# Optimization experiments

Measured on AMD Instinct MI355X. Metric: run time of the kernel, lower is better.

## Reference

```python
import jax, jax.numpy as jnp
import numpy as np

N, E, G = 20000, 320000, 64
IN, ED, H, F, FC, NC = 6, 2, 4, 64, 64, 2
HF = H * F


def _glorot(key, shape):
    fan_in, fan_out = shape[0], shape[-1]
    s = jnp.sqrt(6.0 / (fan_in + fan_out))
    return jax.random.uniform(key, shape, jnp.float32, -s, s)


def setup_inputs() -> dict:
    key = jax.random.key(0)
    ks = jax.random.split(key, 24)
    inp = {
        "x": jax.random.normal(ks[0], (N, IN), jnp.float32),
        "edge_index": jax.random.randint(ks[1], (2, E), 0, N, jnp.int64),
        "edge_attr": jax.random.normal(ks[2], (E, ED), jnp.float32),
        "batch": jnp.sort(jax.random.randint(ks[3], (N,), 0, G, jnp.int64)),
        # layer 0 (GATv2, in=6 -> 4 heads x 64)
        "Wl0": _glorot(ks[4], (IN, HF)), "bl0": jnp.zeros((HF,), jnp.float32),
        "Wr0": _glorot(ks[5], (IN, HF)), "br0": jnp.zeros((HF,), jnp.float32),
        "We0": _glorot(ks[6], (ED, HF)),
        "att0": _glorot(ks[7], (H, F)), "b0": jnp.zeros((HF,), jnp.float32),
        "proj0": _glorot(ks[8], (IN, HF)),  # residual projection 6 -> 256
        # layer 1 (GATv2, in=256 -> 4 heads x 64); residual is identity (256==256)
        "Wl1": _glorot(ks[9], (HF, HF)), "bl1": jnp.zeros((HF,), jnp.float32),
        "Wr1": _glorot(ks[10], (HF, HF)), "br1": jnp.zeros((HF,), jnp.float32),
        "We1": _glorot(ks[11], (ED, HF)),
        "att1": _glorot(ks[12], (H, F)), "b1": jnp.zeros((HF,), jnp.float32),
        # head
        "Wp": _glorot(ks[13], (HF, FC)), "bp": jnp.zeros((FC,), jnp.float32),
        "Wc": _glorot(ks[14], (FC, NC)), "bc": jnp.zeros((NC,), jnp.float32),
    }
    return inp


def _add_self_loops_mean(src, dst, eattr):
    # PyG add_self_loops(fill_value='mean'): self-loop attr = mean of incoming edge_attr
    s = jax.ops.segment_sum(eattr, dst, num_segments=N)
    c = jax.ops.segment_sum(jnp.ones((eattr.shape[0], 1), eattr.dtype), dst, num_segments=N)
    loop_attr = s / jnp.maximum(c, 1.0)
    idx = jnp.arange(N, dtype=src.dtype)
    return (jnp.concatenate([src, idx]), jnp.concatenate([dst, idx]),
            jnp.concatenate([eattr, loop_attr], axis=0))


def _gatv2(x, src, dst, ee, Wl, bl, Wr, br, att, bias):
    # ee: precomputed edge projection [E2, H, F]
    xl = (x @ Wl + bl).reshape(N, H, F)   # source transform
    xr = (x @ Wr + br).reshape(N, H, F)   # target transform
    m = jax.nn.leaky_relu(xl[src] + xr[dst] + ee, 0.2)   # [E2, H, F]
    logits = jnp.einsum('ehf,hf->eh', m, att)            # [E2, H]
    mx = jax.ops.segment_max(logits, dst, num_segments=N)
    ex = jnp.exp(logits - mx[dst])
    den = jax.ops.segment_sum(ex, dst, num_segments=N)
    alpha = ex / den[dst]                                 # scatter-softmax over dst
    out = jax.ops.segment_sum(xl[src] * alpha[:, :, None], dst, num_segments=N)
    return out.reshape(N, HF) + bias


def reference(x, edge_index, edge_attr, batch,
              Wl0, bl0, Wr0, br0, We0, att0, b0, proj0,
              Wl1, bl1, Wr1, br1, We1, att1, b1,
              Wp, bp, Wc, bc):
    src, dst, eattr = _add_self_loops_mean(edge_index[0], edge_index[1], edge_attr)
    # layer 0 (residual: projected input); dropout is a no-op in eval mode
    h = _gatv2(x, src, dst, (eattr @ We0).reshape(-1, H, F), Wl0, bl0, Wr0, br0, att0, b0)
    x1 = jax.nn.elu(h) + x @ proj0
    # layer 1 (residual: identity)
    h = _gatv2(x1, src, dst, (eattr @ We1).reshape(-1, H, F), Wl1, bl1, Wr1, br1, att1, b1)
    x2 = jax.nn.elu(h) + x1
    # pre-pool MLP + global mean pool over graphs + classifier
    z = jax.nn.elu(x2 @ Wp + bp)                           # [N, FC]
    gs = jax.ops.segment_sum(z, batch, num_segments=G)
    gc = jax.ops.segment_sum(jnp.ones((N, 1), z.dtype), batch, num_segments=G)
    pooled = gs / jnp.maximum(gc, 1.0)                     # [G, FC]
    return pooled @ Wc + bc                                # [G, NC]
```

## Files before the change

kernel.cpp:

```cpp
#include <hip/hip_runtime.h>
#include <math.h>

#define NN   20000
#define NE   320000
#define NG   64
#define INF_ 6
#define EDF  2
#define NH   4
#define FD   64
#define HF   256
#define FCD  64
#define NCD  2
#define CAP  64

#define ZB   ((NN + 255) / 256)
#define WCB  512
#define L0B  ((NN + 3) / 4)

typedef short bf16x8 __attribute__((ext_vector_type(8)));
typedef float f32x4  __attribute__((ext_vector_type(4)));

static __device__ __forceinline__ unsigned short f2bf(float f) {
  unsigned u = __float_as_uint(f);
  unsigned r = 0x7fffu + ((u >> 16) & 1u);
  return (unsigned short)((u + r) >> 16);
}
static __device__ __forceinline__ float4 bf2f4(uint2 p) {
  float4 v;
  v.x = __uint_as_float(p.x << 16);
  v.y = __uint_as_float(p.x & 0xffff0000u);
  v.z = __uint_as_float(p.y << 16);
  v.w = __uint_as_float(p.y & 0xffff0000u);
  return v;
}


__global__ __launch_bounds__(256) void k_init(
    int* __restrict__ cnt, float* __restrict__ gpool,
    const float* __restrict__ Wl1, const float* __restrict__ Wr1,
    unsigned short* __restrict__ Wsw,
    const float* __restrict__ x,
    const float* __restrict__ Wl0, const float* __restrict__ bl0,
    const float* __restrict__ Wr0, const float* __restrict__ br0,
    unsigned short* __restrict__ xlb, unsigned short* __restrict__ xrb) {
  int b = blockIdx.x;
  int t = threadIdx.x;
  if (b < ZB) {
    int i = b * 256 + t;
    if (i < NN) cnt[i] = 0;
  } else if (b == ZB) {
    for (int i = t; i < NG * FCD; i += 256) gpool[i] = 0.f;
  } else if (b < ZB + 1 + WCB) {
    int id = (b - ZB - 1) * 256 + t;
    int j = id & 7, lane = (id >> 3) & 63, kk8 = (id >> 9) & 7, ntg = id >> 12;
    int n = ntg * 16 + (lane & 15);
    int k = kk8 * 32 + (lane >> 4) * 8 + j;
    float v = (n < 256) ? Wl1[k * 256 + n] : Wr1[k * 256 + (n - 256)];
    Wsw[id] = f2bf(v);
  } else {
    int w = t >> 6, lane = t & 63;
    int n = (b - ZB - 1 - WCB) * 4 + w;
    if (n >= NN) return;
    int cb = lane << 2;
    float4 al = *(const float4*)&bl0[cb];
    float4 ar = *(const float4*)&br0[cb];
#pragma unroll
    for (int k = 0; k < INF_; ++k) {
      float xv = x[n * INF_ + k];
      float4 wl = *(const float4*)&Wl0[k * HF + cb];
      float4 wr = *(const float4*)&Wr0[k * HF + cb];
      al.x = fmaf(xv, wl.x, al.x); al.y = fmaf(xv, wl.y, al.y);
      al.z = fmaf(xv, wl.z, al.z); al.w = fmaf(xv, wl.w, al.w);
      ar.x = fmaf(xv, wr.x, ar.x); ar.y = fmaf(xv, wr.y, ar.y);
      ar.z = fmaf(xv, wr.z, ar.z); ar.w = fmaf(xv, wr.w, ar.w);
    }
    uint2 pk;
    pk.x = (unsigned)f2bf(al.x) | ((unsigned)f2bf(al.y) << 16);
    pk.y = (unsigned)f2bf(al.z) | ((unsigned)f2bf(al.w) << 16);
    *(uint2*)&xlb[(size_t)n * HF + cb] = pk;
    uint2 pr;
    pr.x = (unsigned)f2bf(ar.x) | ((unsigned)f2bf(ar.y) << 16);
    pr.y = (unsigned)f2bf(ar.z) | ((unsigned)f2bf(ar.w) << 16);
    *(uint2*)&xrb[(size_t)n * HF + cb] = pr;
  }
}


__global__ void k_scatter(const int* __restrict__ ei, const float* __restrict__ ea,
                          int* __restrict__ cnt, uint2* __restrict__ rec) {
  int i = blockIdx.x * blockDim.x + threadIdx.x;
  if (i >= NE) return;
  int s = ei[i], d = ei[NE + i];
  float2 a = *(const float2*)&ea[2 * i];
  int pos = atomicAdd(&cnt[d], 1);
  if (pos < CAP)
    rec[(size_t)d * CAP + pos] = make_uint2((unsigned)(s * 512),
                                            (unsigned)f2bf(a.x) | ((unsigned)f2bf(a.y) << 16));
}


__global__ __launch_bounds__(256) void k_l1_mfma(
    const unsigned short* __restrict__ x1b,
    const unsigned short* __restrict__ Wsw,
    const float* __restrict__ bl, const float* __restrict__ br,
    unsigned short* __restrict__ xlb, unsigned short* __restrict__ xrb) {
  __shared__ unsigned short so[64][264];
  int t = threadIdx.x;
  int row0 = blockIdx.x * 64;
  int w = t >> 6, lane = t & 63;
  int quad = lane >> 4, ln = lane & 15;
  int y = blockIdx.y;
  const float* bias = y ? br : bl;
  unsigned short* dst = y ? xrb : xlb;

  int arow = row0 + w * 16 + ln; if (arow >= NN) arow = NN - 1;
  const unsigned short* aptr = x1b + (size_t)arow * HF + quad * 8;

  f32x4 acc[16];
#pragma unroll
  for (int i = 0; i < 16; ++i) acc[i] = (f32x4){0.f, 0.f, 0.f, 0.f};

  for (int kk8 = 0; kk8 < 8; ++kk8) {
    bf16x8 af = *(const bf16x8*)(aptr + kk8 * 32);
#pragma unroll
    for (int nt = 0; nt < 16; ++nt) {
      bf16x8 bfr = *(const bf16x8*)&Wsw[(size_t)((((y * 16 + nt) * 8 + kk8) * 64) + lane) * 8];
      acc[nt] = __builtin_amdgcn_mfma_f32_16x16x32_bf16(af, bfr, acc[nt], 0, 0, 0);
    }
  }
#pragma unroll
  for (int nt = 0; nt < 16; ++nt) {
    float bv = bias[nt * 16 + ln];
#pragma unroll
    for (int rg = 0; rg < 4; ++rg)
      so[w * 16 + quad * 4 + rg][nt * 16 + ln] = f2bf(acc[nt][rg] + bv);
  }
  __syncthreads();
#pragma unroll
  for (int i = 0; i < 8; ++i) {
    int idx = i * 256 + t;
    int row = idx >> 5, c8 = idx & 31;
    int grow = row0 + row;
    if (grow < NN)
      *(uint4*)&dst[(size_t)grow * HF + c8 * 8] = *(const uint4*)&so[row][c8 * 8];
  }
}


template <bool L0>
__global__ __launch_bounds__(256) void k_agg(
    const unsigned short* __restrict__ xlb, const unsigned short* xrb_,
    const int* __restrict__ cnt, const uint2* __restrict__ rec,
    const float* __restrict__ att, const float* __restrict__ We,
    const float* __restrict__ bias,
    const float* __restrict__ x, const float* __restrict__ proj0,
    unsigned short* __restrict__ x1bout,
    const unsigned short* __restrict__ x1bin, unsigned short* x2bout) {
  int wid = (blockIdx.x * 256 + threadIdx.x) >> 6;
  if (wid >= NN) return;
  int lane = threadIdx.x & 63;
  int n = wid;
  int cb = lane << 2;

  float4 xr4 = bf2f4(*(const uint2*)&xrb_[(size_t)n * HF + cb]);
  float4 at4 = *(const float4*)&att[cb];
  float4 w04 = *(const float4*)&We[cb];
  float4 w14 = *(const float4*)&We[HF + cb];

  int nreal = min(cnt[n], CAP);
  const uint2* recn = rec + (size_t)n * CAP;
  const char* xlbase = (const char*)xlb + (size_t)(cb * 2);

  float a0s = 0.f, a1s = 0.f;
  for (int e = lane; e < nreal; e += 64) {
    uint2 r = recn[e];
    a0s += __uint_as_float(r.y << 16);
    a1s += __uint_as_float(r.y & 0xffff0000u);
  }
#pragma unroll
  for (int o = 32; o; o >>= 1) {
    a0s += __shfl_xor(a0s, o, 64);
    a1s += __shfl_xor(a1s, o, 64);
  }
  float im = 1.0f / fmaxf((float)nreal, 1.0f);
  float a0m = a0s * im, a1m = a1s * im;

  uint2 ps = *(const uint2*)(xlbase + (unsigned)(n * 512));
  float4 vS = bf2f4(ps);
  float tS;
  {
    float4 mm;
    mm.x = vS.x + fmaf(a0m, w04.x, fmaf(a1m, w14.x, xr4.x));
    mm.y = vS.y + fmaf(a0m, w04.y, fmaf(a1m, w14.y, xr4.y));
    mm.z = vS.z + fmaf(a0m, w04.z, fmaf(a1m, w14.z, xr4.z));
    mm.w = vS.w + fmaf(a0m, w04.w, fmaf(a1m, w14.w, xr4.w));
    mm.x = fmaxf(mm.x, 0.2f * mm.x);
    mm.y = fmaxf(mm.y, 0.2f * mm.y);
    mm.z = fmaxf(mm.z, 0.2f * mm.z);
    mm.w = fmaxf(mm.w, 0.2f * mm.w);
    float tt = mm.x * at4.x;
    tt = fmaf(mm.y, at4.y, tt);
    tt = fmaf(mm.z, at4.z, tt);
    tt = fmaf(mm.w, at4.w, tt);
    tt += __shfl_xor(tt, 1, 64);
    tt += __shfl_xor(tt, 2, 64);
    tt += __shfl_xor(tt, 4, 64);
    tt += __shfl_xor(tt, 8, 64);
    tS = tt;
  }
  float den = 1.f;
  float4 acc = vS;

  if (nreal > 0) {
    int lastE = nreal - 1;
    for (int e0 = 0; e0 < nreal; e0 += 4) {
      uint2 r4[4], p4[4];
#pragma unroll
      for (int i = 0; i < 4; ++i)
        r4[i] = recn[min(e0 + i, lastE)];
#pragma unroll
      for (int i = 0; i < 4; ++i)
        p4[i] = *(const uint2*)(xlbase + r4[i].x);

      float t4[4];
#pragma unroll
      for (int i = 0; i < 4; ++i) {
        float4 vC = bf2f4(p4[i]);
        float a0 = __uint_as_float(r4[i].y << 16);
        float a1 = __uint_as_float(r4[i].y & 0xffff0000u);
        float4 mm;
        mm.x = vC.x + fmaf(a0, w04.x, fmaf(a1, w14.x, xr4.x));
        mm.y = vC.y + fmaf(a0, w04.y, fmaf(a1, w14.y, xr4.y));
        mm.z = vC.z + fmaf(a0, w04.z, fmaf(a1, w14.z, xr4.z));
        mm.w = vC.w + fmaf(a0, w04.w, fmaf(a1, w14.w, xr4.w));
        mm.x = fmaxf(mm.x, 0.2f * mm.x);
        mm.y = fmaxf(mm.y, 0.2f * mm.y);
        mm.z = fmaxf(mm.z, 0.2f * mm.z);
        mm.w = fmaxf(mm.w, 0.2f * mm.w);
        float tt = mm.x * at4.x;
        tt = fmaf(mm.y, at4.y, tt);
        tt = fmaf(mm.z, at4.z, tt);
        tt = fmaf(mm.w, at4.w, tt);
        t4[i] = tt;
      }
#pragma unroll
      for (int o = 1; o <= 8; o <<= 1) {
#pragma unroll
        for (int i = 0; i < 4; ++i) t4[i] += __shfl_xor(t4[i], o, 64);
      }
#pragma unroll
      for (int i = 0; i < 4; ++i) {
        float w = (e0 + i <= lastE) ? __expf(fminf(t4[i] - tS, 80.f)) : 0.f;
        float4 vC = bf2f4(p4[i]);
        den += w;
        acc.x = fmaf(w, vC.x, acc.x);
        acc.y = fmaf(w, vC.y, acc.y);
        acc.z = fmaf(w, vC.z, acc.z);
        acc.w = fmaf(w, vC.w, acc.w);
      }
    }
  }

  float inv = 1.0f / den;
  float4 b4 = *(const float4*)&bias[cb];
  float4 o;
  o.x = fmaf(acc.x, inv, b4.x);
  o.y = fmaf(acc.y, inv, b4.y);
  o.z = fmaf(acc.z, inv, b4.z);
  o.w = fmaf(acc.w, inv, b4.w);
  o.x = (o.x > 0.f) ? o.x : expm1f(o.x);
  o.y = (o.y > 0.f) ? o.y : expm1f(o.y);
  o.z = (o.z > 0.f) ? o.z : expm1f(o.z);
  o.w = (o.w > 0.f) ? o.w : expm1f(o.w);

  if (L0) {
    float4 rr = make_float4(0.f, 0.f, 0.f, 0.f);
#pragma unroll
    for (int k = 0; k < INF_; ++k) {
      float xv = x[n * INF_ + k];
      float4 p = *(const float4*)&proj0[k * HF + cb];
      rr.x = fmaf(xv, p.x, rr.x);
      rr.y = fmaf(xv, p.y, rr.y);
      rr.z = fmaf(xv, p.z, rr.z);
      rr.w = fmaf(xv, p.w, rr.w);
    }
    o.x += rr.x; o.y += rr.y; o.z += rr.z; o.w += rr.w;
    uint2 pk;
    pk.x = (unsigned)f2bf(o.x) | ((unsigned)f2bf(o.y) << 16);
    pk.y = (unsigned)f2bf(o.z) | ((unsigned)f2bf(o.w) << 16);
    *(uint2*)&x1bout[(size_t)n * HF + cb] = pk;
  } else {
    float4 x1v = bf2f4(*(const uint2*)&x1bin[(size_t)n * HF + cb]);
    o.x += x1v.x; o.y += x1v.y; o.z += x1v.z; o.w += x1v.w;
    uint2 pk;
    pk.x = (unsigned)f2bf(o.x) | ((unsigned)f2bf(o.y) << 16);
    pk.y = (unsigned)f2bf(o.z) | ((unsigned)f2bf(o.w) << 16);
    *(uint2*)&x2bout[(size_t)n * HF + cb] = pk;
  }
}


__global__ __launch_bounds__(256) void k_pool(
    const unsigned short* __restrict__ x2b, const float* __restrict__ Wp,
    const float* __restrict__ bp, const int* __restrict__ batch,
    float* __restrict__ gpool) {
  __shared__ float xs[32 * HF];
  __shared__ int gid_s[32];
  int t = threadIdx.x;
  int row0 = blockIdx.x * 32;
  const uint4* s4 = (const uint4*)(x2b + (size_t)row0 * HF);
#pragma unroll
  for (int i = 0; i < 4; ++i) {
    int idx = i * 256 + t;
    uint4 p = s4[idx];
    int base = idx * 8;
    float4 lo = bf2f4(make_uint2(p.x, p.y));
    float4 hi = bf2f4(make_uint2(p.z, p.w));
    *(float4*)&xs[base] = lo;
    *(float4*)&xs[base + 4] = hi;
  }
  if (t < 32) gid_s[t] = batch[row0 + t];
  __syncthreads();
  int j = t & 63, rg = t >> 6;
  float acc[8];
#pragma unroll
  for (int rr = 0; rr < 8; ++rr) acc[rr] = 0.f;
  for (int k4 = 0; k4 < HF / 4; ++k4) {
    float w0 = Wp[(k4 * 4 + 0) * FCD + j];
    float w1 = Wp[(k4 * 4 + 1) * FCD + j];
    float w2 = Wp[(k4 * 4 + 2) * FCD + j];
    float w3 = Wp[(k4 * 4 + 3) * FCD + j];
#pragma unroll
    for (int rr = 0; rr < 8; ++rr) {
      float4 xv = *(const float4*)&xs[(rg * 8 + rr) * HF + k4 * 4];
      acc[rr] = fmaf(xv.x, w0, acc[rr]);
      acc[rr] = fmaf(xv.y, w1, acc[rr]);
      acc[rr] = fmaf(xv.z, w2, acc[rr]);
      acc[rr] = fmaf(xv.w, w3, acc[rr]);
    }
  }
  float b = bp[j];
  int gprev = gid_s[rg * 8];
  float run = 0.f;
#pragma unroll
  for (int rr = 0; rr < 8; ++rr) {
    float a = acc[rr] + b;
    float z = (a > 0.f) ? a : expm1f(a);
    int g = gid_s[rg * 8 + rr];
    if (g != gprev) {
      atomicAdd(&gpool[gprev * FCD + j], run);
      run = 0.f; gprev = g;
    }
    run += z;
  }
  atomicAdd(&gpool[gprev * FCD + j], run);
}


__global__ void k_head(const float* __restrict__ gpool, const int* __restrict__ batch,
                       const float* __restrict__ Wc, const float* __restrict__ bc,
                       float* __restrict__ out) {
  int t = threadIdx.x;
  int g = t >> 1, k = t & 1;
  int lo = 0, hi = NN;
  while (lo < hi) { int mid = (lo + hi) >> 1; if (batch[mid] < g) lo = mid + 1; else hi = mid; }
  int c0 = lo;
  lo = 0; hi = NN;
  while (lo < hi) { int mid = (lo + hi) >> 1; if (batch[mid] < g + 1) lo = mid + 1; else hi = mid; }
  int c1 = lo;
  float inv = 1.0f / fmaxf((float)(c1 - c0), 1.0f);
  float a = bc[k];
  for (int j = 0; j < FCD; ++j)
    a = fmaf(gpool[g * FCD + j] * inv, Wc[j * NCD + k], a);
  out[g * NCD + k] = a;
}


extern "C" void kernel_launch(void* const* d_in, const int* in_sizes, int n_in,
                              void* d_out, int out_size, void* d_ws, size_t ws_size,
                              hipStream_t stream) {
  const float* x    = (const float*)d_in[0];
  const int*   ei   = (const int*)d_in[1];
  const float* ea   = (const float*)d_in[2];
  const int*   batch= (const int*)d_in[3];
  const float* Wl0  = (const float*)d_in[4];
  const float* bl0  = (const float*)d_in[5];
  const float* Wr0  = (const float*)d_in[6];
  const float* br0  = (const float*)d_in[7];
  const float* We0  = (const float*)d_in[8];
  const float* att0 = (const float*)d_in[9];
  const float* b0   = (const float*)d_in[10];
  const float* proj0= (const float*)d_in[11];
  const float* Wl1  = (const float*)d_in[12];
  const float* bl1  = (const float*)d_in[13];
  const float* Wr1  = (const float*)d_in[14];
  const float* br1  = (const float*)d_in[15];
  const float* We1  = (const float*)d_in[16];
  const float* att1 = (const float*)d_in[17];
  const float* b1   = (const float*)d_in[18];
  const float* Wp   = (const float*)d_in[19];
  const float* bp   = (const float*)d_in[20];
  const float* Wc   = (const float*)d_in[21];
  const float* bc   = (const float*)d_in[22];
  float* out = (float*)d_out;

  char* ws = (char*)d_ws;
  size_t off = 0;
  int*   cnt    = (int*)(ws + off);   off += (NN * 4 + 15) / 16 * 16;
  uint2* rec    = (uint2*)(ws + off); off += (size_t)NN * CAP * 8;
  unsigned short* xlb = (unsigned short*)(ws + off); off += (size_t)NN * HF * 2;
  unsigned short* xrb = (unsigned short*)(ws + off); off += (size_t)NN * HF * 2;
  unsigned short* x1b = (unsigned short*)(ws + off); off += (size_t)NN * HF * 2;
  float* gpool  = (float*)(ws + off); off += NG * FCD * 4;
  unsigned short* Wsw = (unsigned short*)(ws + off); off += 512 * 256 * 2;
  unsigned short* x2b = xrb;
  (void)ws_size; (void)in_sizes; (void)n_in; (void)out_size;

  k_init<<<ZB + 1 + WCB + L0B, 256, 0, stream>>>(
      cnt, gpool, Wl1, Wr1, Wsw, x, Wl0, bl0, Wr0, br0, xlb, xrb);

  k_scatter<<<(NE + 255) / 256, 256, 0, stream>>>(ei, ea, cnt, rec);

  k_agg<true><<<(NN * 64 + 255) / 256, 256, 0, stream>>>(
      xlb, xrb, cnt, rec, att0, We0, b0, x, proj0, x1b, nullptr, nullptr);

  k_l1_mfma<<<dim3((NN + 63) / 64, 2), 256, 0, stream>>>(x1b, Wsw, bl1, br1, xlb, xrb);
  k_agg<false><<<(NN * 64 + 255) / 256, 256, 0, stream>>>(
      xlb, xrb, cnt, rec, att1, We1, b1, nullptr, nullptr, nullptr, x1b, x2b);

  k_pool<<<NN / 32, 256, 0, stream>>>(x2b, Wp, bp, batch, gpool);
  k_head<<<1, 128, 0, stream>>>(gpool, batch, Wc, bc, out);
}
```

Before: 266.1 us.

## Fuse edge-attr mean into softmax loop, pack FP32 math, count graph sizes in pool

The aggregation kernel no longer makes a separate pass over the edge records to compute the self-loop mean attribute. It accumulates that sum inside the main softmax loop and handles the self-loop term afterwards, which lets the max-shift subtraction be dropped. The edge loop is unrolled from 4 to 8 edges per iteration and uses two-wide float vectors so the compiler can emit packed FP32 instructions, and a dummy early record load is kept alive with an empty asm statement. The pooling kernel now counts nodes per graph with atomics, replacing the binary searches in the head kernel. Dropping the max-shift makes the exponent depend only on the clamp at 80, which risks overflow or precision differences for large logits.

New measurement: 304.4 us. +14.4%, slower.

```diff
diff --git a/kernel.cpp b/kernel.cpp
--- a/kernel.cpp
+++ b/kernel.cpp
@@ -19,6 +19,7 @@
 
 typedef short bf16x8 __attribute__((ext_vector_type(8)));
 typedef float f32x4  __attribute__((ext_vector_type(4)));
+typedef float f32x2  __attribute__((ext_vector_type(2)));
 
 static __device__ __forceinline__ unsigned short f2bf(float f) {
   unsigned u = __float_as_uint(f);
@@ -33,10 +34,16 @@
   v.w = __uint_as_float(p.y & 0xffff0000u);
   return v;
 }
+static __device__ __forceinline__ f32x2 bflo2(unsigned u) {
+  f32x2 v;
+  v.x = __uint_as_float(u << 16);
+  v.y = __uint_as_float(u & 0xffff0000u);
+  return v;
+}
 
 
 __global__ __launch_bounds__(256) void k_init(
-    int* __restrict__ cnt, float* __restrict__ gpool,
+    int* __restrict__ cnt, float* __restrict__ gpool, int* __restrict__ gcnt,
     const float* __restrict__ Wl1, const float* __restrict__ Wr1,
     unsigned short* __restrict__ Wsw,
     const float* __restrict__ x,
@@ -50,6 +57,7 @@
     if (i < NN) cnt[i] = 0;
   } else if (b == ZB) {
     for (int i = t; i < NG * FCD; i += 256) gpool[i] = 0.f;
+    if (t < NG) gcnt[t] = 0;
   } else if (b < ZB + 1 + WCB) {
     int id = (b - ZB - 1) * 256 + t;
     int j = id & 7, lane = (id >> 3) & 63, kk8 = (id >> 9) & 7, ntg = id >> 12;
@@ -161,130 +169,121 @@
   int lane = threadIdx.x & 63;
   int n = wid;
   int cb = lane << 2;
+  unsigned cbb = (unsigned)(cb << 1);
+
+  const char* xlbase = (const char*)xlb;
+  uint2 ps = *(const uint2*)(xlbase + ((unsigned)(n * 512) + cbb));
 
   float4 xr4 = bf2f4(*(const uint2*)&xrb_[(size_t)n * HF + cb]);
   float4 at4 = *(const float4*)&att[cb];
   float4 w04 = *(const float4*)&We[cb];
   float4 w14 = *(const float4*)&We[HF + cb];
+  f32x2 xrA = {xr4.x, xr4.y}, xrB = {xr4.z, xr4.w};
+  f32x2 atA = {at4.x, at4.y}, atB = {at4.z, at4.w};
+  f32x2 w0A = {w04.x, w04.y}, w0B = {w04.z, w04.w};
+  f32x2 w1A = {w14.x, w14.y}, w1B = {w14.z, w14.w};
 
   int nreal = min(cnt[n], CAP);
+  int lastE = nreal - 1;
   const uint2* recn = rec + (size_t)n * CAP;
-  const char* xlbase = (const char*)xlb + (size_t)(cb * 2);
-
-  float a0s = 0.f, a1s = 0.f;
-  for (int e = lane; e < nreal; e += 64) {
-    uint2 r = recn[e];
-    a0s += __uint_as_float(r.y << 16);
-    a1s += __uint_as_float(r.y & 0xffff0000u);
-  }
-#pragma unroll
-  for (int o = 32; o; o >>= 1) {
-    a0s += __shfl_xor(a0s, o, 64);
-    a1s += __shfl_xor(a1s, o, 64);
-  }
+  uint2 pre = recn[lane];
+
+  f32x2 accA = {0.f, 0.f}, accB = {0.f, 0.f};
+  float den = 0.f, a0s = 0.f, a1s = 0.f;
+
+  for (int e0 = 0; e0 < nreal; e0 += 8) {
+    uint2 r8[8], p8[8];
+#pragma unroll
+    for (int i = 0; i < 8; ++i)
+      r8[i] = recn[min(e0 + i, lastE)];
+#pragma unroll
+    for (int i = 0; i < 8; ++i)
+      p8[i] = *(const uint2*)(xlbase + (r8[i].x + cbb));
+
+    float t8[8];
+#pragma unroll
+    for (int i = 0; i < 8; ++i) {
+      float a0 = __uint_as_float(r8[i].y << 16);
+      float a1 = __uint_as_float(r8[i].y & 0xffff0000u);
+      if (e0 + i <= lastE) { a0s += a0; a1s += a1; }
+      f32x2 a0v = {a0, a0}, a1v = {a1, a1};
+      f32x2 mA = a1v * w1A + xrA; mA = a0v * w0A + mA;
+      f32x2 mB = a1v * w1B + xrB; mB = a0v * w0B + mB;
+      mA = mA + bflo2(p8[i].x);
+      mB = mB + bflo2(p8[i].y);
+      mA.x = fmaxf(mA.x, 0.2f * mA.x);
+      mA.y = fmaxf(mA.y, 0.2f * mA.y);
+      mB.x = fmaxf(mB.x, 0.2f * mB.x);
+      mB.y = fmaxf(mB.y, 0.2f * mB.y);
+      f32x2 d = mA * atA;
+      d = mB * atB + d;
+      t8[i] = d.x + d.y;
+    }
+#pragma unroll
+    for (int o = 1; o <= 8; o <<= 1) {
+#pragma unroll
+      for (int i = 0; i < 8; ++i) t8[i] += __shfl_xor(t8[i], o, 64);
+    }
+#pragma unroll
+    for (int i = 0; i < 8; ++i) {
+      float w = (e0 + i <= lastE) ? __expf(fminf(t8[i], 80.f)) : 0.f;
+      den += w;
+      f32x2 wv = {w, w};
+      accA = wv * bflo2(p8[i].x) + accA;
+      accB = wv * bflo2(p8[i].y) + accB;
+    }
+  }
+
   float im = 1.0f / fmaxf((float)nreal, 1.0f);
   float a0m = a0s * im, a1m = a1s * im;
-
-  uint2 ps = *(const uint2*)(xlbase + (unsigned)(n * 512));
-  float4 vS = bf2f4(ps);
-  float tS;
+  f32x2 vSA = bflo2(ps.x), vSB = bflo2(ps.y);
   {
-    float4 mm;
-    mm.x = vS.x + fmaf(a0m, w04.x, fmaf(a1m, w14.x, xr4.x));
-    mm.y = vS.y + fmaf(a0m, w04.y, fmaf(a1m, w14.y, xr4.y));
-    mm.z = vS.z + fmaf(a0m, w04.z, fmaf(a1m, w14.z, xr4.z));
-    mm.w = vS.w + fmaf(a0m, w04.w, fmaf(a1m, w14.w, xr4.w));
-    mm.x = fmaxf(mm.x, 0.2f * mm.x);
-    mm.y = fmaxf(mm.y, 0.2f * mm.y);
-    mm.z = fmaxf(mm.z, 0.2f * mm.z);
-    mm.w = fmaxf(mm.w, 0.2f * mm.w);
-    float tt = mm.x * at4.x;
-    tt = fmaf(mm.y, at4.y, tt);
-    tt = fmaf(mm.z, at4.z, tt);
-    tt = fmaf(mm.w, at4.w, tt);
-    tt += __shfl_xor(tt, 1, 64);
-    tt += __shfl_xor(tt, 2, 64);
-    tt += __shfl_xor(tt, 4, 64);
-    tt += __shfl_xor(tt, 8, 64);
-    tS = tt;
-  }
-  float den = 1.f;
-  float4 acc = vS;
-
-  if (nreal > 0) {
-    int lastE = nreal - 1;
-    for (int e0 = 0; e0 < nreal; e0 += 4) {
-      uint2 r4[4], p4[4];
-#pragma unroll
-      for (int i = 0; i < 4; ++i)
-        r4[i] = recn[min(e0 + i, lastE)];
-#pragma unroll
-      for (int i = 0; i < 4; ++i)
-        p4[i] = *(const uint2*)(xlbase + r4[i].x);
-
-      float t4[4];
-#pragma unroll
-      for (int i = 0; i < 4; ++i) {
-        float4 vC = bf2f4(p4[i]);
-        float a0 = __uint_as_float(r4[i].y << 16);
-        float a1 = __uint_as_float(r4[i].y & 0xffff0000u);
-        float4 mm;
-        mm.x = vC.x + fmaf(a0, w04.x, fmaf(a1, w14.x, xr4.x));
-        mm.y = vC.y + fmaf(a0, w04.y, fmaf(a1, w14.y, xr4.y));
-        mm.z = vC.z + fmaf(a0, w04.z, fmaf(a1, w14.z, xr4.z));
-        mm.w = vC.w + fmaf(a0, w04.w, fmaf(a1, w14.w, xr4.w));
-        mm.x = fmaxf(mm.x, 0.2f * mm.x);
-        mm.y = fmaxf(mm.y, 0.2f * mm.y);
-        mm.z = fmaxf(mm.z, 0.2f * mm.z);
-        mm.w = fmaxf(mm.w, 0.2f * mm.w);
-        float tt = mm.x * at4.x;
-        tt = fmaf(mm.y, at4.y, tt);
-        tt = fmaf(mm.z, at4.z, tt);
-        tt = fmaf(mm.w, at4.w, tt);
-        t4[i] = tt;
-      }
-#pragma unroll
-      for (int o = 1; o <= 8; o <<= 1) {
-#pragma unroll
-        for (int i = 0; i < 4; ++i) t4[i] += __shfl_xor(t4[i], o, 64);
-      }
-#pragma unroll
-      for (int i = 0; i < 4; ++i) {
-        float w = (e0 + i <= lastE) ? __expf(fminf(t4[i] - tS, 80.f)) : 0.f;
-        float4 vC = bf2f4(p4[i]);
-        den += w;
-        acc.x = fmaf(w, vC.x, acc.x);
-        acc.y = fmaf(w, vC.y, acc.y);
-        acc.z = fmaf(w, vC.z, acc.z);
-        acc.w = fmaf(w, vC.w, acc.w);
-      }
-    }
+    f32x2 a0v = {a0m, a0m}, a1v = {a1m, a1m};
+    f32x2 mA = a1v * w1A + xrA; mA = a0v * w0A + mA;
+    f32x2 mB = a1v * w1B + xrB; mB = a0v * w0B + mB;
+    mA = mA + vSA; mB = mB + vSB;
+    mA.x = fmaxf(mA.x, 0.2f * mA.x);
+    mA.y = fmaxf(mA.y, 0.2f * mA.y);
+    mB.x = fmaxf(mB.x, 0.2f * mB.x);
+    mB.y = fmaxf(mB.y, 0.2f * mB.y);
+    f32x2 d = mA * atA;
+    d = mB * atB + d;
+    float tS = d.x + d.y;
+    tS += __shfl_xor(tS, 1, 64);
+    tS += __shfl_xor(tS, 2, 64);
+    tS += __shfl_xor(tS, 4, 64);
+    tS += __shfl_xor(tS, 8, 64);
+    float wS = __expf(fminf(tS, 80.f));
+    den += wS;
+    f32x2 wv = {wS, wS};
+    accA = wv * vSA + accA;
+    accB = wv * vSB + accB;
   }
 
   float inv = 1.0f / den;
   float4 b4 = *(const float4*)&bias[cb];
   float4 o;
-  o.x = fmaf(acc.x, inv, b4.x);
-  o.y = fmaf(acc.y, inv, b4.y);
-  o.z = fmaf(acc.z, inv, b4.z);
-  o.w = fmaf(acc.w, inv, b4.w);
+  o.x = fmaf(accA.x, inv, b4.x);
+  o.y = fmaf(accA.y, inv, b4.y);
+  o.z = fmaf(accB.x, inv, b4.z);
+  o.w = fmaf(accB.y, inv, b4.w);
   o.x = (o.x > 0.f) ? o.x : expm1f(o.x);
   o.y = (o.y > 0.f) ? o.y : expm1f(o.y);
   o.z = (o.z > 0.f) ? o.z : expm1f(o.z);
   o.w = (o.w > 0.f) ? o.w : expm1f(o.w);
 
   if (L0) {
-    float4 rr = make_float4(0.f, 0.f, 0.f, 0.f);
+    f32x2 rA = {0.f, 0.f}, rB = {0.f, 0.f};
 #pragma unroll
     for (int k = 0; k < INF_; ++k) {
       float xv = x[n * INF_ + k];
       float4 p = *(const float4*)&proj0[k * HF + cb];
-      rr.x = fmaf(xv, p.x, rr.x);
-      rr.y = fmaf(xv, p.y, rr.y);
-      rr.z = fmaf(xv, p.z, rr.z);
-      rr.w = fmaf(xv, p.w, rr.w);
-    }
-    o.x += rr.x; o.y += rr.y; o.z += rr.z; o.w += rr.w;
+      f32x2 xvv = {xv, xv};
+      f32x2 pA = {p.x, p.y}, pB = {p.z, p.w};
+      rA = xvv * pA + rA;
+      rB = xvv * pB + rB;
+    }
+    o.x += rA.x; o.y += rA.y; o.z += rB.x; o.w += rB.y;
     uint2 pk;
     pk.x = (unsigned)f2bf(o.x) | ((unsigned)f2bf(o.y) << 16);
     pk.y = (unsigned)f2bf(o.z) | ((unsigned)f2bf(o.w) << 16);
@@ -297,13 +296,14 @@
     pk.y = (unsigned)f2bf(o.z) | ((unsigned)f2bf(o.w) << 16);
     *(uint2*)&x2bout[(size_t)n * HF + cb] = pk;
   }
+  asm volatile("" :: "v"(pre.x), "v"(pre.y));
 }
 
 
 __global__ __launch_bounds__(256) void k_pool(
     const unsigned short* __restrict__ x2b, const float* __restrict__ Wp,
     const float* __restrict__ bp, const int* __restrict__ batch,
-    float* __restrict__ gpool) {
+    float* __restrict__ gpool, int* __restrict__ gcnt) {
   __shared__ float xs[32 * HF];
   __shared__ int gid_s[32];
   int t = threadIdx.x;
@@ -342,6 +342,7 @@
   float b = bp[j];
   int gprev = gid_s[rg * 8];
   float run = 0.f;
+  int rcnt = 0;
 #pragma unroll
   for (int rr = 0; rr < 8; ++rr) {
     float a = acc[rr] + b;
@@ -349,27 +350,24 @@
     int g = gid_s[rg * 8 + rr];
     if (g != gprev) {
       atomicAdd(&gpool[gprev * FCD + j], run);
-      run = 0.f; gprev = g;
-    }
-    run += z;
+      if (j == 0) atomicAdd(&gcnt[gprev], rcnt);
+      run = 0.f; rcnt = 0; gprev = g;
+    }
+    run += z; ++rcnt;
   }
   atomicAdd(&gpool[gprev * FCD + j], run);
-}
-
-
-__global__ void k_head(const float* __restrict__ gpool, const int* __restrict__ batch,
+  if (j == 0) atomicAdd(&gcnt[gprev], rcnt);
+}
+
+
+__global__ void k_head(const float* __restrict__ gpool, const int* __restrict__ gcnt,
                        const float* __restrict__ Wc, const float* __restrict__ bc,
                        float* __restrict__ out) {
   int t = threadIdx.x;
   int g = t >> 1, k = t & 1;
-  int lo = 0, hi = NN;
-  while (lo < hi) { int mid = (lo + hi) >> 1; if (batch[mid] < g) lo = mid + 1; else hi = mid; }
-  int c0 = lo;
-  lo = 0; hi = NN;
-  while (lo < hi) { int mid = (lo + hi) >> 1; if (batch[mid] < g + 1) lo = mid + 1; else hi = mid; }
-  int c1 = lo;
-  float inv = 1.0f / fmaxf((float)(c1 - c0), 1.0f);
+  float inv = 1.0f / fmaxf((float)gcnt[g], 1.0f);
   float a = bc[k];
+#pragma unroll
   for (int j = 0; j < FCD; ++j)
     a = fmaf(gpool[g * FCD + j] * inv, Wc[j * NCD + k], a);
   out[g * NCD + k] = a;
@@ -413,11 +411,12 @@
   unsigned short* x1b = (unsigned short*)(ws + off); off += (size_t)NN * HF * 2;
   float* gpool  = (float*)(ws + off); off += NG * FCD * 4;
   unsigned short* Wsw = (unsigned short*)(ws + off); off += 512 * 256 * 2;
+  int*   gcnt   = (int*)(ws + off);   off += (NG * 4 + 15) / 16 * 16;
   unsigned short* x2b = xrb;
   (void)ws_size; (void)in_sizes; (void)n_in; (void)out_size;
 
   k_init<<<ZB + 1 + WCB + L0B, 256, 0, stream>>>(
-      cnt, gpool, Wl1, Wr1, Wsw, x, Wl0, bl0, Wr0, br0, xlb, xrb);
+      cnt, gpool, gcnt, Wl1, Wr1, Wsw, x, Wl0, bl0, Wr0, br0, xlb, xrb);
 
   k_scatter<<<(NE + 255) / 256, 256, 0, stream>>>(ei, ea, cnt, rec);
 
@@ -428,6 +427,6 @@
   k_agg<false><<<(NN * 64 + 255) / 256, 256, 0, stream>>>(
       xlb, xrb, cnt, rec, att1, We1, b1, nullptr, nullptr, nullptr, x1b, x2b);
 
-  k_pool<<<NN / 32, 256, 0, stream>>>(x2b, Wp, bp, batch, gpool);
-  k_head<<<1, 128, 0, stream>>>(gpool, batch, Wc, bc, out);
-}
+  k_pool<<<NN / 32, 256, 0, stream>>>(x2b, Wp, bp, batch, gpool, gcnt);
+  k_head<<<1, 128, 0, stream>>>(gpool, gcnt, Wc, bc, out);
+}
```
